# Kernel tuning notes

Hardware: AMD Instinct MI355X
Metric: run time of the kernel (lower is better)

## Reference

```python
import jax, jax.numpy as jnp
import numpy as np
from jax import lax

B, T, N, H, NC = 2, 8, 512, 64, 10
NEG = -1e9
LN_EPS = 1e-5


def _gatv2(x, mask, Wl, Wr, att, b):
    # GATv2Conv (PyG semantics, eval mode): e_ij = att . leaky_relu(Wr x_i + Wl x_j),
    # softmax over source nodes j with self-loops, out_i = sum_j alpha_ij * (Wl x_j).
    # x: (B, N, Fin); mask: (N, N) bool adjacency incl. self-loops; att: (heads, C).
    heads, C = att.shape
    Bn, Nn, _ = x.shape
    xl = (x @ Wl).reshape(Bn, Nn, heads, C)  # source transform
    xr = (x @ Wr).reshape(Bn, Nn, heads, C)  # target transform
    s = jax.nn.leaky_relu(xr[:, :, None] + xl[:, None, :], 0.2)  # (B, Ni, Nj, h, C)
    e = jnp.einsum('bijhc,hc->bijh', s, att)
    e = jnp.where(mask[None, :, :, None], e, NEG)
    alpha = jax.nn.softmax(e, axis=2)  # softmax over neighbors j
    out = jnp.einsum('bijh,bjhc->bihc', alpha, xl)
    return out.reshape(Bn, Nn, heads * C) + b


def _gru_layer(x, Wih, Whh, bih, bhh):
    # torch nn.GRU single layer, batch_first; x: (B, T, Hin)
    h0 = jnp.zeros((x.shape[0], Whh.shape[0]), x.dtype)
    def step(h, xt):
        gi = xt @ Wih + bih
        gh = h @ Whh + bhh
        ir, iz, inn = jnp.split(gi, 3, axis=-1)
        hr, hz, hn = jnp.split(gh, 3, axis=-1)
        r = jax.nn.sigmoid(ir + hr)
        z = jax.nn.sigmoid(iz + hz)
        n = jnp.tanh(inn + r * hn)
        hnew = (1.0 - z) * n + z * h
        return hnew, hnew
    _, ys = lax.scan(step, h0, jnp.swapaxes(x, 0, 1))
    return jnp.swapaxes(ys, 0, 1)


def setup_inputs() -> dict:
    key = jax.random.key(0)
    ks = jax.random.split(key, 20)
    def rn(i, shape, s=0.1):
        return jax.random.normal(ks[i], shape, jnp.float32) * s
    x_seq = jax.random.normal(ks[0], (B, T, N, 1), jnp.float32)
    a = jax.random.uniform(ks[1], (N, N))
    up = jnp.triu((a > 0.95).astype(jnp.float32), 1)
    static_adj = up + up.T  # sparse symmetric 0/1 static graph
    dyn_W = jax.random.normal(ks[2], (N, N), jnp.float32)
    reg_lambda = jnp.array([0.05], jnp.float32)
    return {
        'x_seq': x_seq, 'static_adj': static_adj, 'dyn_W': dyn_W, 'reg_lambda': reg_lambda,
        'g1_Wl': rn(3, (1, H)), 'g1_Wr': rn(4, (1, H)), 'g1_att': rn(5, (4, H // 4)), 'g1_b': jnp.zeros(H),
        'g2_Wl': rn(6, (H, H)), 'g2_Wr': rn(7, (H, H)), 'g2_att': rn(8, (1, H)), 'g2_b': jnp.zeros(H),
        'gru_Wih0': rn(9, (H, 3 * H)), 'gru_Whh0': rn(10, (H, 3 * H)), 'gru_bih0': jnp.zeros(3 * H), 'gru_bhh0': jnp.zeros(3 * H),
        'gru_Wih1': rn(11, (H, 3 * H)), 'gru_Whh1': rn(12, (H, 3 * H)), 'gru_bih1': jnp.zeros(3 * H), 'gru_bhh1': jnp.zeros(3 * H),
        'attn_W': rn(13, (H, 1)), 'attn_b': jnp.zeros(1),
        'cls_W1': rn(14, (H, H)), 'cls_b1': jnp.zeros(H), 'ln_g': jnp.ones(H), 'ln_b': jnp.zeros(H),
        'cls_W2': rn(15, (H, NC)), 'cls_b2': jnp.zeros(NC),
    }


def reference(x_seq, static_adj, dyn_W, reg_lambda,
              g1_Wl, g1_Wr, g1_att, g1_b, g2_Wl, g2_Wr, g2_att, g2_b,
              gru_Wih0, gru_Whh0, gru_bih0, gru_bhh0,
              gru_Wih1, gru_Whh1, gru_bih1, gru_bhh1,
              attn_W, attn_b, cls_W1, cls_b1, ln_g, ln_b, cls_W2, cls_b2):
    Bn, Tn, Nn, _ = x_seq.shape
    lam = jnp.maximum(reg_lambda[0], 0.01)
    t = jnp.arange(Tn, dtype=x_seq.dtype)
    gts = jnp.exp(-lam * t)  # gating values per timestep
    dyn = jax.nn.relu(dyn_W + dyn_W.T)
    fused = gts[:, None, None] * static_adj + (1.0 - gts)[:, None, None] * dyn  # (T, N, N)
    masks = (fused > 0) | jnp.eye(Nn, dtype=bool)[None]  # edge set + self-loops

    def step(carry, inp):
        xt, mask = inp  # xt: (B, N, 1)
        h = jax.nn.elu(_gatv2(xt, mask, g1_Wl, g1_Wr, g1_att, g1_b))
        h = jax.nn.elu(_gatv2(h, mask, g2_Wl, g2_Wr, g2_att, g2_b))
        return carry, h.mean(axis=1)  # (B, H) graph readout

    _, reps = lax.scan(step, 0.0, (jnp.swapaxes(x_seq, 0, 1), masks))
    h_seq = jnp.swapaxes(reps, 0, 1)  # (B, T, H)

    gru_out = _gru_layer(h_seq, gru_Wih0, gru_Whh0, gru_bih0, gru_bhh0)
    gru_out = _gru_layer(gru_out, gru_Wih1, gru_Whh1, gru_bih1, gru_bhh1)

    att_scores = jax.nn.softmax((gru_out @ attn_W + attn_b)[..., 0], axis=1)  # (B, T)
    final = jnp.einsum('bt,bth->bh', att_scores, gru_out)

    z = final @ cls_W1 + cls_b1
    mu = jnp.mean(z, axis=-1, keepdims=True)
    var = jnp.var(z, axis=-1, keepdims=True)
    z = (z - mu) / jnp.sqrt(var + LN_EPS) * ln_g + ln_b
    z = jax.nn.gelu(z, approximate=False)
    logits = z @ cls_W2 + cls_b2
    return logits, gts, att_scores
```

## Files before the change

### kernel.cpp

```cpp
#include <hip/hip_runtime.h>
#include <math.h>

#define BB 2
#define TT 8
#define NN 512
#define HH 64
#define NC 10

typedef unsigned char uchar;

__device__ __forceinline__ float elu1(float v){ return v > 0.f ? v : expm1f(v); }
__device__ __forceinline__ float sigm(float v){ return 1.f/(1.f+expf(-v)); }

__global__ __launch_bounds__(256) void k_mask(
    const float* __restrict__ dW, const float* __restrict__ sadj,
    uchar* __restrict__ M0, uchar* __restrict__ M1,
    float* __restrict__ hseq,
    const float* __restrict__ att1, const float* __restrict__ Wr1,
    const float* __restrict__ Wl1, float* __restrict__ AB,
    const float* __restrict__ Whh0, const float* __restrict__ Wih1,
    const float* __restrict__ Whh1, float4* __restrict__ WT4)
{
    __shared__ float tr[64][65];
    int bx = blockIdx.x, by = blockIdx.y;
    int tid = threadIdx.x;
    if (blockIdx.z == 1){
        int idx = (by*8 + bx)*256 + tid;
        if (idx < 3*4096){
            int m = idx >> 12, r = idx & 4095;
            int gg = r >> 6, k = r & 63;
            const float* W = (m == 0) ? Whh0 : (m == 1) ? Wih1 : Whh1;
            float4 o;
            o.x = W[k*192 + gg];
            o.y = W[k*192 + 64 + gg];
            o.z = W[k*192 + 128 + gg];
            o.w = 0.f;
            WT4[(size_t)m*4096 + r] = o;
        }
        return;
    }
    int i0 = by*64, j0 = bx*64;
    #pragma unroll
    for (int q = 0; q < 4; ++q){
        int r = (tid >> 4) + 16*q, c4 = tid & 15;
        float4 v = *(const float4*)&dW[(size_t)(j0+r)*NN + i0 + 4*c4];
        tr[r][4*c4+0] = v.x; tr[r][4*c4+1] = v.y;
        tr[r][4*c4+2] = v.z; tr[r][4*c4+3] = v.w;
    }
    __syncthreads();
    #pragma unroll
    for (int q = 0; q < 4; ++q){
        int row = (tid >> 4) + 16*q, c4 = tid & 15;
        int i = i0 + row, j = j0 + 4*c4;
        float4 d  = *(const float4*)&dW[(size_t)i*NN + j];
        float4 sa = *(const float4*)&sadj[(size_t)i*NN + j];
        uchar4 m0, m1;
        float dd0 = d.x + tr[4*c4+0][row];
        float dd1 = d.y + tr[4*c4+1][row];
        float dd2 = d.z + tr[4*c4+2][row];
        float dd3 = d.w + tr[4*c4+3][row];
        m0.x = (sa.x > 0.f) || (i == j+0);
        m0.y = (sa.y > 0.f) || (i == j+1);
        m0.z = (sa.z > 0.f) || (i == j+2);
        m0.w = (sa.w > 0.f) || (i == j+3);
        m1.x = m0.x || (dd0 > 0.f);
        m1.y = m0.y || (dd1 > 0.f);
        m1.z = m0.z || (dd2 > 0.f);
        m1.w = m0.w || (dd3 > 0.f);
        *(uchar4*)&M0[(size_t)i*NN + j] = m0;
        *(uchar4*)&M1[(size_t)i*NN + j] = m1;
    }
    int flat = (by*8 + bx)*256 + tid;
    if (flat < BB*TT*HH) hseq[flat] = 0.f;
    if (bx == 0 && by == 0 && tid < 8){
        int h = tid & 3;
        const float* W = (tid < 4) ? Wr1 : Wl1;
        float s = 0.f;
        for (int c = 0; c < 16; ++c) s += att1[h*16+c]*W[h*16+c];
        AB[tid] = s;
    }
}

__global__ __launch_bounds__(256) void k_gat1f(
    const float* __restrict__ x_seq, const uchar* __restrict__ M0,
    const uchar* __restrict__ M1,
    const float* __restrict__ Wl, const float* __restrict__ Wr,
    const float* __restrict__ att, const float* __restrict__ bias,
    const float* __restrict__ AB,
    const float* __restrict__ Wl2, const float* __restrict__ Wr2,
    const float* __restrict__ att2,
    float* __restrict__ xl2, float* __restrict__ xr2,
    float* __restrict__ ui, float* __restrict__ vj)
{
    __shared__ float x_s[NN];
    __shared__ float S_s[4][4];
    __shared__ float h_s[4][HH];
    __shared__ float Wl2_s[64*64];
    __shared__ float Wr2_s[64*64];
    int bt = blockIdx.y; int t = bt % TT;
    int i0 = blockIdx.x * 4;
    int tid = threadIdx.x;
    int il = tid >> 6, jl = tid & 63;
    int i = i0 + il;
    const uchar* M = t ? M1 : M0;
    ((float2*)x_s)[tid] = ((const float2*)(x_seq + bt*NN))[tid];
    #pragma unroll
    for (int q = 0; q < 4; ++q){
        int idx = q*256 + tid;
        ((float4*)Wl2_s)[idx] = ((const float4*)Wl2)[idx];
        ((float4*)Wr2_s)[idx] = ((const float4*)Wr2)[idx];
    }
    __syncthreads();
    float xi = x_s[i];
    const uchar* Mrow = M + (size_t)i*NN;
    float xj[8], msk[8];
    #pragma unroll
    for (int jj = 0; jj < 8; ++jj){
        int j = jj*64 + jl;
        xj[jj] = x_s[j];
        msk[jj] = Mrow[j] ? 1.f : 0.f;
    }
    float sw[4] = {0,0,0,0}, swx[4] = {0,0,0,0};
    for (int h = 0; h < 4; ++h){
        float acc[8] = {0,0,0,0,0,0,0,0};
        #pragma unroll
        for (int c = 0; c < 16; ++c){
            int hc = h*16 + c;
            float wl = Wl[hc];
            float q  = 0.4f * att[hc];
            float pr = xi * Wr[hc];
            #pragma unroll
            for (int jj = 0; jj < 8; ++jj){
                float s = fmaf(xj[jj], wl, pr);
                acc[jj] = fmaf(q, fabsf(s), acc[jj]);
            }
        }
        float lin = 0.6f * xi * AB[h];
        float al6 = 0.6f * AB[4+h];
        #pragma unroll
        for (int jj = 0; jj < 8; ++jj){
            float e = acc[jj] + fmaf(al6, xj[jj], lin);
            float w = msk[jj] * __expf(e);
            sw[h] += w;
            swx[h] = fmaf(w, xj[jj], swx[h]);
        }
    }
    #pragma unroll
    for (int off = 32; off; off >>= 1){
        #pragma unroll
        for (int h = 0; h < 4; ++h){
            sw[h]  += __shfl_down(sw[h],  off);
            swx[h] += __shfl_down(swx[h], off);
        }
    }
    if (jl == 0){
        #pragma unroll
        for (int h = 0; h < 4; ++h) S_s[il][h] = swx[h] / sw[h];
    }
    __syncthreads();
    {
        int hc = tid & 63, row = tid >> 6;
        float v = S_s[row][hc >> 4] * Wl[hc] + bias[hc];
        h_s[row][hc] = elu1(v);
    }
    __syncthreads();
    {
        int c = tid & 63, row = tid >> 6;
        float al = 0.f, ar = 0.f;
        #pragma unroll 8
        for (int k = 0; k < 64; ++k){
            float hv = h_s[row][k];
            al = fmaf(hv, Wl2_s[k*64 + c], al);
            ar = fmaf(hv, Wr2_s[k*64 + c], ar);
        }
        size_t ridx = (size_t)(bt*NN + i0 + row);
        xl2[ridx*HH + c] = al;
        xr2[ridx*HH + c] = ar;
        float a2 = att2[c];
        float pu = a2 * ar, pv = a2 * al;
        #pragma unroll
        for (int off = 32; off; off >>= 1){
            pu += __shfl_down(pu, off);
            pv += __shfl_down(pv, off);
        }
        if (c == 0){ ui[ridx] = pu; vj[ridx] = pv; }
    }
}

__global__ __launch_bounds__(512) void k_gat2(
    const float* __restrict__ xl2, const float* __restrict__ xr2,
    const uchar* __restrict__ M0, const uchar* __restrict__ M1,
    const float* __restrict__ att, const float* __restrict__ ui,
    const float* __restrict__ vj, const float* __restrict__ bias,
    float* __restrict__ hseq)
{
    __shared__ float xl_s[256][68];
    __shared__ float wT_s[256][36];
    __shared__ float v_s[256];
    __shared__ float z_s[32];

    int bt = blockIdx.y, t = bt & 7;
    int i0 = blockIdx.x * 32;
    int base = bt * NN;
    int tid = threadIdx.x;
    const uchar* M = t ? M1 : M0;

    int ig = __builtin_amdgcn_readfirstlane(tid >> 6);
    int jg = tid & 63;
    int ln = jg;
    int ig2 = ln >> 3, cg2 = ln & 7;

    const float* xrp0 = xr2 + (size_t)(base + i0 + ig*4 + 0)*HH;
    const float* xrp1 = xr2 + (size_t)(base + i0 + ig*4 + 1)*HH;
    const float* xrp2 = xr2 + (size_t)(base + i0 + ig*4 + 2)*HH;
    const float* xrp3 = xr2 + (size_t)(base + i0 + ig*4 + 3)*HH;
    float u0 = 0.6f*ui[base + i0 + ig*4 + 0];
    float u1 = 0.6f*ui[base + i0 + ig*4 + 1];
    float u2 = 0.6f*ui[base + i0 + ig*4 + 2];
    float u3 = 0.6f*ui[base + i0 + ig*4 + 3];

    float zreg[4] = {0.f,0.f,0.f,0.f};
    float acc[4][8];
    #pragma unroll
    for (int a = 0; a < 4; ++a)
        #pragma unroll
        for (int r = 0; r < 8; ++r) acc[a][r] = 0.f;

    for (int tile = 0; tile < 2; ++tile){
        int j0 = tile * 256;
        __syncthreads();
        #pragma unroll
        for (int q = 0; q < 8; ++q){
            int idx = q*512 + tid;
            int row = idx >> 4, c4 = idx & 15;
            ((float4*)&xl_s[row][0])[c4] = ((const float4*)&xl2[(size_t)(base+j0+row)*HH])[c4];
        }
        if (tid < 256) v_s[tid] = vj[base + j0 + tid];
        __syncthreads();
        float e[4][4];
        #pragma unroll
        for (int jj = 0; jj < 4; ++jj){
            float vv = 0.6f * v_s[jj*64 + jg];
            e[0][jj] = u0 + vv; e[1][jj] = u1 + vv;
            e[2][jj] = u2 + vv; e[3][jj] = u3 + vv;
        }
        #pragma unroll 4
        for (int c4 = 0; c4 < 16; ++c4){
            float4 a4 = *(const float4*)&att[c4*4];
            float qk[4];
            qk[0] = 0.4f*a4.x; qk[1] = 0.4f*a4.y; qk[2] = 0.4f*a4.z; qk[3] = 0.4f*a4.w;
            float rr[4][4];
            *(float4*)rr[0] = *(const float4*)&xrp0[c4*4];
            *(float4*)rr[1] = *(const float4*)&xrp1[c4*4];
            *(float4*)rr[2] = *(const float4*)&xrp2[c4*4];
            *(float4*)rr[3] = *(const float4*)&xrp3[c4*4];
            float xlv[4][4];
            #pragma unroll
            for (int jj = 0; jj < 4; ++jj)
                *(float4*)xlv[jj] = ((const float4*)&xl_s[jj*64+jg][0])[c4];
            #pragma unroll
            for (int jj = 0; jj < 4; ++jj)
                #pragma unroll
                for (int k = 0; k < 4; ++k){
                    float xc = xlv[jj][k];
                    #pragma unroll
                    for (int ii = 0; ii < 4; ++ii)
                        e[ii][jj] = fmaf(qk[k], fabsf(rr[ii][k] + xc), e[ii][jj]);
                }
        }
        #pragma unroll
        for (int jj = 0; jj < 4; ++jj){
            int j = jj*64 + jg;
            const uchar* mp = &M[(size_t)(i0 + ig*4)*NN + j0 + j];
            float w0 = mp[0]      ? __expf(e[0][jj]) : 0.f;
            float w1 = mp[NN]     ? __expf(e[1][jj]) : 0.f;
            float w2 = mp[2*NN]   ? __expf(e[2][jj]) : 0.f;
            float w3 = mp[3*NN]   ? __expf(e[3][jj]) : 0.f;
            zreg[0] += w0; zreg[1] += w1; zreg[2] += w2; zreg[3] += w3;
            float4 wq; wq.x = w0; wq.y = w1; wq.z = w2; wq.w = w3;
            *(float4*)&wT_s[j][ig*4] = wq;
        }
        __syncthreads();
        #pragma unroll 4
        for (int jj = 0; jj < 32; ++jj){
            int j = ig*32 + jj;
            float w4[4], xa[8];
            *(float4*)w4      = *(const float4*)&wT_s[j][ig2*4];
            *(float4*)&xa[0]  = ((const float4*)&xl_s[j][0])[cg2*2+0];
            *(float4*)&xa[4]  = ((const float4*)&xl_s[j][0])[cg2*2+1];
            #pragma unroll
            for (int a = 0; a < 4; ++a)
                #pragma unroll
                for (int r = 0; r < 8; ++r)
                    acc[a][r] = fmaf(w4[a], xa[r], acc[a][r]);
        }
    }
    __syncthreads();
    #pragma unroll
    for (int off = 32; off; off >>= 1){
        #pragma unroll
        for (int ii = 0; ii < 4; ++ii) zreg[ii] += __shfl_down(zreg[ii], off);
    }
    if (jg == 0){
        #pragma unroll
        for (int ii = 0; ii < 4; ++ii) z_s[ig*4+ii] = zreg[ii];
    }
    float* scratch = &xl_s[0][0];
    if (ig > 0){
        #pragma unroll
        for (int a = 0; a < 4; ++a)
            #pragma unroll
            for (int r = 0; r < 8; ++r)
                scratch[(a*8+r)*448 + (ig-1)*64 + ln] = acc[a][r];
    }
    __syncthreads();
    if (ig == 0){
        float pm[8];
        #pragma unroll
        for (int r = 0; r < 8; ++r) pm[r] = 0.f;
        #pragma unroll
        for (int a = 0; a < 4; ++a){
            float rz = 1.f / z_s[ig2*4 + a];
            #pragma unroll
            for (int r = 0; r < 8; ++r){
                float s = acc[a][r];
                #pragma unroll
                for (int w = 0; w < 7; ++w)
                    s += scratch[(a*8+r)*448 + w*64 + ln];
                float h = elu1(s*rz + bias[cg2*8 + r]);
                pm[r] += h;
            }
        }
        #pragma unroll
        for (int off = 32; off >= 8; off >>= 1){
            #pragma unroll
            for (int r = 0; r < 8; ++r) pm[r] += __shfl_down(pm[r], off);
        }
        if (ig2 == 0){
            #pragma unroll
            for (int r = 0; r < 8; ++r)
                atomicAdd(&hseq[bt*HH + cg2*8 + r], pm[r] * (1.f/(float)NN));
        }
    }
}

#define P4 65
__global__ __launch_bounds__(512) void k_gru2(
    const float* __restrict__ hseq, const float* __restrict__ Wih0,
    const float* __restrict__ bih0, const float4* __restrict__ WT4,
    const float* __restrict__ bhh0,
    const float* __restrict__ bih1, const float* __restrict__ bhh1,
    const float* __restrict__ lamp, const float* __restrict__ attn_W,
    const float* __restrict__ attn_b, const float* __restrict__ W1,
    const float* __restrict__ b1, const float* __restrict__ ln_g,
    const float* __restrict__ ln_b, const float* __restrict__ W2,
    const float* __restrict__ b2, float* __restrict__ out)
{
    __shared__ float4 WA[64*P4];
    __shared__ float4 WB[64*P4];
    __shared__ float gi_s[BB*TT*192];
    __shared__ float hs_s[BB*TT*HH];
    __shared__ float y_s[BB*TT*HH];
    __shared__ float sc_s[BB][TT], at_s[BB][TT];
    __shared__ float fin_s[BB][HH], z_s[BB][HH], g_s[BB][HH];
    __shared__ float mu_s[BB], iv_s[BB];
    int tid = threadIdx.x;
    int wave = tid >> 6, lane = tid & 63;
    for (int v = tid; v < 4096; v += 512){
        WA[(v >> 6)*P4 + (v & 63)] = WT4[v];
        WB[(v >> 6)*P4 + (v & 63)] = WT4[4096 + v];
    }
    for (int v = tid; v < BB*TT*HH; v += 512) hs_s[v] = hseq[v];
    __syncthreads();
    #pragma unroll
    for (int o = 0; o < 6; ++o){
        int idx = o*512 + tid;
        int b = idx / 192, g = idx % 192;
        float a = bih0[g];
        const float* hr = &hs_s[b*HH];
        #pragma unroll 8
        for (int k = 0; k < HH; ++k) a = fmaf(hr[k], Wih0[k*192 + g], a);
        gi_s[idx] = a;
    }
    __syncthreads();
    float y[TT];
    float g1r[TT], g1z[TT], g1n[TT];
    if (wave < 2){
        int b = wave;
        float bhr = bhh0[lane], bhz = bhh0[64+lane], bhn = bhh0[128+lane];
        float h = 0.f;
        for (int t = 0; t < TT; ++t){
            float ghr = bhr, ghz = bhz, ghn = bhn;
            #pragma unroll 16
            for (int k = 0; k < 64; ++k){
                float4 w4 = WA[lane*P4 + k];
                float hk = __shfl(h, k);
                ghr = fmaf(w4.x, hk, ghr);
                ghz = fmaf(w4.y, hk, ghz);
                ghn = fmaf(w4.z, hk, ghn);
            }
            const float* gi = &gi_s[(b*TT + t)*192];
            float r = sigm(gi[lane] + ghr);
            float z = sigm(gi[64+lane] + ghz);
            float n = tanhf(gi[128+lane] + r*ghn);
            h = (1.f - z)*n + z*h;
            y[t] = h;
        }
        float bi1r = bih1[lane], bi1z = bih1[64+lane], bi1n = bih1[128+lane];
        #pragma unroll
        for (int t = 0; t < TT; ++t){ g1r[t] = bi1r; g1z[t] = bi1z; g1n[t] = bi1n; }
        #pragma unroll 8
        for (int k = 0; k < 64; ++k){
            float4 w4 = WB[lane*P4 + k];
            #pragma unroll
            for (int t = 0; t < TT; ++t){
                float yk = __shfl(y[t], k);
                g1r[t] = fmaf(w4.x, yk, g1r[t]);
                g1z[t] = fmaf(w4.y, yk, g1z[t]);
                g1n[t] = fmaf(w4.z, yk, g1n[t]);
            }
        }
    }
    __syncthreads();
    if (wave >= 2){
        for (int v = tid - 128; v < 4096; v += 384)
            WA[(v >> 6)*P4 + (v & 63)] = WT4[2*4096 + v];
    }
    __syncthreads();
    if (wave < 2){
        int b = wave;
        float bhr = bhh1[lane], bhz = bhh1[64+lane], bhn = bhh1[128+lane];
        float h = 0.f;
        for (int t = 0; t < TT; ++t){
            float ghr = bhr, ghz = bhz, ghn = bhn;
            #pragma unroll 16
            for (int k = 0; k < 64; ++k){
                float4 w4 = WA[lane*P4 + k];
                float hk = __shfl(h, k);
                ghr = fmaf(w4.x, hk, ghr);
                ghz = fmaf(w4.y, hk, ghz);
                ghn = fmaf(w4.z, hk, ghn);
            }
            float r = sigm(g1r[t] + ghr);
            float z = sigm(g1z[t] + ghz);
            float n = tanhf(g1n[t] + r*ghn);
            h = (1.f - z)*n + z*h;
            y_s[(b*TT + t)*HH + lane] = h;
        }
    }
    __syncthreads();
    float lam = fmaxf(lamp[0], 0.01f);
    if (tid < TT) out[BB*NC + tid] = expf(-lam*(float)tid);
    if (tid < BB*TT){
        int bb = tid >> 3, t = tid & 7;
        float s = attn_b[0];
        const float* r = &y_s[(bb*TT+t)*HH];
        for (int h = 0; h < HH; ++h) s += r[h]*attn_W[h];
        sc_s[bb][t] = s;
    }
    __syncthreads();
    if (tid < BB){
        float mx = -INFINITY;
        for (int t = 0; t < TT; ++t) mx = fmaxf(mx, sc_s[tid][t]);
        float se = 0.f;
        for (int t = 0; t < TT; ++t){ float w = expf(sc_s[tid][t]-mx); at_s[tid][t] = w; se += w; }
        for (int t = 0; t < TT; ++t){
            at_s[tid][t] /= se;
            out[BB*NC + TT + tid*TT + t] = at_s[tid][t];
        }
    }
    __syncthreads();
    if (tid < BB*HH){
        int bb = tid >> 6, h = tid & 63;
        float a = 0.f;
        for (int t = 0; t < TT; ++t) a += at_s[bb][t]*y_s[(bb*TT+t)*HH + h];
        fin_s[bb][h] = a;
    }
    __syncthreads();
    if (tid < BB*HH){
        int bb = tid >> 6, h = tid & 63;
        float a = b1[h];
        for (int k = 0; k < HH; ++k) a += fin_s[bb][k]*W1[k*HH+h];
        z_s[bb][h] = a;
    }
    __syncthreads();
    if (tid < BB){
        float mu = 0.f;
        for (int h = 0; h < HH; ++h) mu += z_s[tid][h];
        mu *= (1.f/HH);
        float v = 0.f;
        for (int h = 0; h < HH; ++h){ float d = z_s[tid][h]-mu; v += d*d; }
        v *= (1.f/HH);
        mu_s[tid] = mu; iv_s[tid] = 1.f/sqrtf(v + 1e-5f);
    }
    __syncthreads();
    if (tid < BB*HH){
        int bb = tid >> 6, h = tid & 63;
        float zn = (z_s[bb][h]-mu_s[bb])*iv_s[bb]*ln_g[h] + ln_b[h];
        g_s[bb][h] = 0.5f*zn*(1.f + erff(zn*0.70710678118654752f));
    }
    __syncthreads();
    if (tid < BB*NC){
        int bb = tid / NC, c = tid % NC;
        float a = b2[c];
        for (int k = 0; k < HH; ++k) a += g_s[bb][k]*W2[k*NC+c];
        out[bb*NC + c] = a;
    }
}

extern "C" void kernel_launch(void* const* d_in, const int* in_sizes, int n_in,
                              void* d_out, int out_size, void* d_ws, size_t ws_size,
                              hipStream_t stream)
{
    const float* x_seq = (const float*)d_in[0];
    const float* sadj  = (const float*)d_in[1];
    const float* dynW  = (const float*)d_in[2];
    const float* lamp  = (const float*)d_in[3];
    const float* g1_Wl = (const float*)d_in[4];
    const float* g1_Wr = (const float*)d_in[5];
    const float* g1_att= (const float*)d_in[6];
    const float* g1_b  = (const float*)d_in[7];
    const float* g2_Wl = (const float*)d_in[8];
    const float* g2_Wr = (const float*)d_in[9];
    const float* g2_att= (const float*)d_in[10];
    const float* g2_b  = (const float*)d_in[11];
    const float* Wih0  = (const float*)d_in[12];
    const float* Whh0  = (const float*)d_in[13];
    const float* bih0  = (const float*)d_in[14];
    const float* bhh0  = (const float*)d_in[15];
    const float* Wih1  = (const float*)d_in[16];
    const float* Whh1  = (const float*)d_in[17];
    const float* bih1  = (const float*)d_in[18];
    const float* bhh1  = (const float*)d_in[19];
    const float* attnW = (const float*)d_in[20];
    const float* attnb = (const float*)d_in[21];
    const float* W1    = (const float*)d_in[22];
    const float* b1    = (const float*)d_in[23];
    const float* lng   = (const float*)d_in[24];
    const float* lnb   = (const float*)d_in[25];
    const float* W2    = (const float*)d_in[26];
    const float* b2    = (const float*)d_in[27];
    float* out = (float*)d_out;

    const int RWS = BB*TT*NN*HH;
    uchar* M0 = (uchar*)d_ws;
    uchar* M1 = M0 + (size_t)NN*NN;
    float* fb = (float*)(M1 + (size_t)NN*NN);
    float* AB   = fb;
    float* ui   = AB   + 16;
    float* vj   = ui   + BB*TT*NN;
    float* xl2  = vj   + BB*TT*NN;
    float* xr2  = xl2  + RWS;
    float* hseq = xr2  + RWS;
    float4* WT4 = (float4*)(hseq + BB*TT*HH);

    k_mask <<<dim3(8,8,2), 256, 0, stream>>>(dynW, sadj, M0, M1, hseq, g1_att, g1_Wr, g1_Wl, AB,
                                             Whh0, Wih1, Whh1, WT4);
    k_gat1f<<<dim3(NN/4, BB*TT), 256, 0, stream>>>(x_seq, M0, M1, g1_Wl, g1_Wr, g1_att, g1_b, AB,
                                                   g2_Wl, g2_Wr, g2_att, xl2, xr2, ui, vj);
    k_gat2 <<<dim3(NN/32, BB*TT), 512, 0, stream>>>(xl2, xr2, M0, M1, g2_att, ui, vj, g2_b, hseq);
    k_gru2 <<<1, 512, 0, stream>>>(hseq, Wih0, bih0, WT4, bhh0, bih1, bhh1,
                                   lamp, attnW, attnb, W1, b1, lng, lnb, W2, b2, out);
}
```

Measured before the change: 222.8 us.

## Split GRU recurrent matvec across two waves with register-resident weights

Each batch's hidden-to-hidden matvec is split across two waves, each holding half of the transposed Whh in registers. The hidden state is now exchanged through LDS rather than shuffles, and partial sums are combined after a block barrier. The layer-1 input projection is computed by all 512 threads reading Wih1 from global memory, instead of inside the two GRU waves. This shortens the serial per-step dependency chain and drops the LDS weight staging, at the cost of two block-wide barriers per timestep and heavier register use.

```diff
diff --git a/kernel.cpp b/kernel.cpp
--- a/kernel.cpp
+++ b/kernel.cpp
@@ -344,11 +344,10 @@
     }
 }
 
-#define P4 65
 __global__ __launch_bounds__(512) void k_gru2(
     const float* __restrict__ hseq, const float* __restrict__ Wih0,
     const float* __restrict__ bih0, const float4* __restrict__ WT4,
-    const float* __restrict__ bhh0,
+    const float* __restrict__ bhh0, const float* __restrict__ Wih1,
     const float* __restrict__ bih1, const float* __restrict__ bhh1,
     const float* __restrict__ lamp, const float* __restrict__ attn_W,
     const float* __restrict__ attn_b, const float* __restrict__ W1,
@@ -356,21 +355,27 @@
     const float* __restrict__ ln_b, const float* __restrict__ W2,
     const float* __restrict__ b2, float* __restrict__ out)
 {
-    __shared__ float4 WA[64*P4];
-    __shared__ float4 WB[64*P4];
     __shared__ float gi_s[BB*TT*192];
     __shared__ float hs_s[BB*TT*HH];
     __shared__ float y_s[BB*TT*HH];
+    __shared__ float h_lds[BB][HH];
+    __shared__ float part_s[BB][2][3][HH];
     __shared__ float sc_s[BB][TT], at_s[BB][TT];
     __shared__ float fin_s[BB][HH], z_s[BB][HH], g_s[BB][HH];
     __shared__ float mu_s[BB], iv_s[BB];
     int tid = threadIdx.x;
     int wave = tid >> 6, lane = tid & 63;
-    for (int v = tid; v < 4096; v += 512){
-        WA[(v >> 6)*P4 + (v & 63)] = WT4[v];
-        WB[(v >> 6)*P4 + (v & 63)] = WT4[4096 + v];
+    int gb = wave >> 1, half = wave & 1;
+    bool gruw = (wave < 4);
+
+    float4 Wreg[32];
+    if (gruw){
+        const float4* src = WT4 + (size_t)lane*64 + half*32;
+        #pragma unroll
+        for (int kk = 0; kk < 32; ++kk) Wreg[kk] = src[kk];
     }
     for (int v = tid; v < BB*TT*HH; v += 512) hs_s[v] = hseq[v];
+    if (tid < BB*HH) h_lds[tid >> 6][tid & 63] = 0.f;
     __syncthreads();
     #pragma unroll
     for (int o = 0; o < 6; ++o){
@@ -383,72 +388,101 @@
         gi_s[idx] = a;
     }
     __syncthreads();
-    float y[TT];
-    float g1r[TT], g1z[TT], g1n[TT];
-    if (wave < 2){
-        int b = wave;
-        float bhr = bhh0[lane], bhz = bhh0[64+lane], bhn = bhh0[128+lane];
-        float h = 0.f;
+    {
+        float bhr = 0.f, bhz = 0.f, bhn = 0.f;
+        if (gruw && half == 0){ bhr = bhh0[lane]; bhz = bhh0[64+lane]; bhn = bhh0[128+lane]; }
         for (int t = 0; t < TT; ++t){
-            float ghr = bhr, ghz = bhz, ghn = bhn;
-            #pragma unroll 16
-            for (int k = 0; k < 64; ++k){
-                float4 w4 = WA[lane*P4 + k];
-                float hk = __shfl(h, k);
-                ghr = fmaf(w4.x, hk, ghr);
-                ghz = fmaf(w4.y, hk, ghz);
-                ghn = fmaf(w4.z, hk, ghn);
+            if (gruw){
+                float hh[32];
+                #pragma unroll
+                for (int q = 0; q < 8; ++q)
+                    *(float4*)&hh[q*4] = *(const float4*)&h_lds[gb][half*32 + q*4];
+                float ar0=0,ar1=0,az0=0,az1=0,an0=0,an1=0;
+                #pragma unroll
+                for (int kk = 0; kk < 32; kk += 2){
+                    ar0 = fmaf(Wreg[kk].x,   hh[kk],   ar0);
+                    az0 = fmaf(Wreg[kk].y,   hh[kk],   az0);
+                    an0 = fmaf(Wreg[kk].z,   hh[kk],   an0);
+                    ar1 = fmaf(Wreg[kk+1].x, hh[kk+1], ar1);
+                    az1 = fmaf(Wreg[kk+1].y, hh[kk+1], az1);
+                    an1 = fmaf(Wreg[kk+1].z, hh[kk+1], an1);
+                }
+                part_s[gb][half][0][lane] = ar0 + ar1;
+                part_s[gb][half][1][lane] = az0 + az1;
+                part_s[gb][half][2][lane] = an0 + an1;
             }
-            const float* gi = &gi_s[(b*TT + t)*192];
-            float r = sigm(gi[lane] + ghr);
-            float z = sigm(gi[64+lane] + ghz);
-            float n = tanhf(gi[128+lane] + r*ghn);
-            h = (1.f - z)*n + z*h;
-            y[t] = h;
-        }
-        float bi1r = bih1[lane], bi1z = bih1[64+lane], bi1n = bih1[128+lane];
-        #pragma unroll
-        for (int t = 0; t < TT; ++t){ g1r[t] = bi1r; g1z[t] = bi1z; g1n[t] = bi1n; }
+            __syncthreads();
+            if (gruw && half == 0){
+                float ghr = part_s[gb][0][0][lane] + part_s[gb][1][0][lane] + bhr;
+                float ghz = part_s[gb][0][1][lane] + part_s[gb][1][1][lane] + bhz;
+                float ghn = part_s[gb][0][2][lane] + part_s[gb][1][2][lane] + bhn;
+                const float* gi = &gi_s[(gb*TT + t)*192];
+                float r = sigm(gi[lane] + ghr);
+                float z = sigm(gi[64+lane] + ghz);
+                float n = tanhf(gi[128+lane] + r*ghn);
+                float hn = (1.f - z)*n + z*h_lds[gb][lane];
+                h_lds[gb][lane] = hn;
+                y_s[(gb*TT + t)*HH + lane] = hn;
+            }
+            __syncthreads();
+        }
+    }
+    if (gruw){
+        const float4* src = WT4 + 2*4096 + (size_t)lane*64 + half*32;
+        #pragma unroll
+        for (int kk = 0; kk < 32; ++kk) Wreg[kk] = src[kk];
+    }
+    #pragma unroll
+    for (int o = 0; o < 6; ++o){
+        int idx = o*512 + tid;
+        int b = idx / 192, g = idx % 192;
+        float a = bih1[g];
+        const float* yr = &y_s[b*HH];
         #pragma unroll 8
-        for (int k = 0; k < 64; ++k){
-            float4 w4 = WB[lane*P4 + k];
-            #pragma unroll
-            for (int t = 0; t < TT; ++t){
-                float yk = __shfl(y[t], k);
-                g1r[t] = fmaf(w4.x, yk, g1r[t]);
-                g1z[t] = fmaf(w4.y, yk, g1z[t]);
-                g1n[t] = fmaf(w4.z, yk, g1n[t]);
+        for (int k = 0; k < HH; ++k) a = fmaf(yr[k], Wih1[k*192 + g], a);
+        gi_s[idx] = a;
+    }
+    if (tid < BB*HH) h_lds[tid >> 6][tid & 63] = 0.f;
+    __syncthreads();
+    {
+        float bhr = 0.f, bhz = 0.f, bhn = 0.f;
+        if (gruw && half == 0){ bhr = bhh1[lane]; bhz = bhh1[64+lane]; bhn = bhh1[128+lane]; }
+        for (int t = 0; t < TT; ++t){
+            if (gruw){
+                float hh[32];
+                #pragma unroll
+                for (int q = 0; q < 8; ++q)
+                    *(float4*)&hh[q*4] = *(const float4*)&h_lds[gb][half*32 + q*4];
+                float ar0=0,ar1=0,az0=0,az1=0,an0=0,an1=0;
+                #pragma unroll
+                for (int kk = 0; kk < 32; kk += 2){
+                    ar0 = fmaf(Wreg[kk].x,   hh[kk],   ar0);
+                    az0 = fmaf(Wreg[kk].y,   hh[kk],   az0);
+                    an0 = fmaf(Wreg[kk].z,   hh[kk],   an0);
+                    ar1 = fmaf(Wreg[kk+1].x, hh[kk+1], ar1);
+                    az1 = fmaf(Wreg[kk+1].y, hh[kk+1], az1);
+                    an1 = fmaf(Wreg[kk+1].z, hh[kk+1], an1);
+                }
+                part_s[gb][half][0][lane] = ar0 + ar1;
+                part_s[gb][half][1][lane] = az0 + az1;
+                part_s[gb][half][2][lane] = an0 + an1;
             }
-        }
-    }
-    __syncthreads();
-    if (wave >= 2){
-        for (int v = tid - 128; v < 4096; v += 384)
-            WA[(v >> 6)*P4 + (v & 63)] = WT4[2*4096 + v];
-    }
-    __syncthreads();
-    if (wave < 2){
-        int b = wave;
-        float bhr = bhh1[lane], bhz = bhh1[64+lane], bhn = bhh1[128+lane];
-        float h = 0.f;
-        for (int t = 0; t < TT; ++t){
-            float ghr = bhr, ghz = bhz, ghn = bhn;
-            #pragma unroll 16
-            for (int k = 0; k < 64; ++k){
-                float4 w4 = WA[lane*P4 + k];
-                float hk = __shfl(h, k);
-                ghr = fmaf(w4.x, hk, ghr);
-                ghz = fmaf(w4.y, hk, ghz);
-                ghn = fmaf(w4.z, hk, ghn);
+            __syncthreads();
+            if (gruw && half == 0){
+                float ghr = part_s[gb][0][0][lane] + part_s[gb][1][0][lane] + bhr;
+                float ghz = part_s[gb][0][1][lane] + part_s[gb][1][1][lane] + bhz;
+                float ghn = part_s[gb][0][2][lane] + part_s[gb][1][2][lane] + bhn;
+                const float* gi = &gi_s[(gb*TT + t)*192];
+                float r = sigm(gi[lane] + ghr);
+                float z = sigm(gi[64+lane] + ghz);
+                float n = tanhf(gi[128+lane] + r*ghn);
+                float hn = (1.f - z)*n + z*h_lds[gb][lane];
+                h_lds[gb][lane] = hn;
+                y_s[(gb*TT + t)*HH + lane] = hn;
             }
-            float r = sigm(g1r[t] + ghr);
-            float z = sigm(g1z[t] + ghz);
-            float n = tanhf(g1n[t] + r*ghn);
-            h = (1.f - z)*n + z*h;
-            y_s[(b*TT + t)*HH + lane] = h;
-        }
-    }
-    __syncthreads();
+            __syncthreads();
+        }
+    }
     float lam = fmaxf(lamp[0], 0.01f);
     if (tid < TT) out[BB*NC + tid] = expf(-lam*(float)tid);
     if (tid < BB*TT){
@@ -559,6 +593,6 @@
     k_gat1f<<<dim3(NN/4, BB*TT), 256, 0, stream>>>(x_seq, M0, M1, g1_Wl, g1_Wr, g1_att, g1_b, AB,
                                                    g2_Wl, g2_Wr, g2_att, xl2, xr2, ui, vj);
     k_gat2 <<<dim3(NN/32, BB*TT), 512, 0, stream>>>(xl2, xr2, M0, M1, g2_att, ui, vj, g2_b, hseq);
-    k_gru2 <<<1, 512, 0, stream>>>(hseq, Wih0, bih0, WT4, bhh0, bih1, bhh1,
+    k_gru2 <<<1, 512, 0, stream>>>(hseq, Wih0, bih0, WT4, bhh0, Wih1, bih1, bhh1,
                                    lamp, attnW, attnb, W1, b1, lng, lnb, W2, b2, out);
 }
```

Result: no change. 223.2 us (+0.2%).

## Hold GRU recurrent weights in registers and compute layer-1 input gates block-wide

Applied to the files above, without the earlier changes.

The GRU kernel now keeps each lane's 64x3 recurrent weight slice in VGPRs, loaded directly from a re-transposed global buffer, instead of reading float4 weights from padded LDS on every step. The layer-1 input projection is no longer done by two waves with shuffles. All 512 threads compute it from y_s using Wih1 straight from global memory, and the prep kernel no longer transposes Wih1. This targets LDS traffic and idle waves in the serial GRU tail, at the cost of about 192 live registers per lane and possible spilling.

```diff
diff --git a/kernel.cpp b/kernel.cpp
--- a/kernel.cpp
+++ b/kernel.cpp
@@ -18,18 +18,18 @@
     float* __restrict__ hseq,
     const float* __restrict__ att1, const float* __restrict__ Wr1,
     const float* __restrict__ Wl1, float* __restrict__ AB,
-    const float* __restrict__ Whh0, const float* __restrict__ Wih1,
-    const float* __restrict__ Whh1, float4* __restrict__ WT4)
+    const float* __restrict__ Whh0, const float* __restrict__ Whh1,
+    float4* __restrict__ WT4)
 {
     __shared__ float tr[64][65];
     int bx = blockIdx.x, by = blockIdx.y;
     int tid = threadIdx.x;
     if (blockIdx.z == 1){
         int idx = (by*8 + bx)*256 + tid;
-        if (idx < 3*4096){
+        if (idx < 2*4096){
             int m = idx >> 12, r = idx & 4095;
-            int gg = r >> 6, k = r & 63;
-            const float* W = (m == 0) ? Whh0 : (m == 1) ? Wih1 : Whh1;
+            int k = r >> 6, gg = r & 63;
+            const float* W = m ? Whh1 : Whh0;
             float4 o;
             o.x = W[k*192 + gg];
             o.y = W[k*192 + 64 + gg];
@@ -344,11 +344,10 @@
     }
 }
 
-#define P4 65
 __global__ __launch_bounds__(512) void k_gru2(
     const float* __restrict__ hseq, const float* __restrict__ Wih0,
     const float* __restrict__ bih0, const float4* __restrict__ WT4,
-    const float* __restrict__ bhh0,
+    const float* __restrict__ bhh0, const float* __restrict__ Wih1,
     const float* __restrict__ bih1, const float* __restrict__ bhh1,
     const float* __restrict__ lamp, const float* __restrict__ attn_W,
     const float* __restrict__ attn_b, const float* __restrict__ W1,
@@ -356,8 +355,6 @@
     const float* __restrict__ ln_b, const float* __restrict__ W2,
     const float* __restrict__ b2, float* __restrict__ out)
 {
-    __shared__ float4 WA[64*P4];
-    __shared__ float4 WB[64*P4];
     __shared__ float gi_s[BB*TT*192];
     __shared__ float hs_s[BB*TT*HH];
     __shared__ float y_s[BB*TT*HH];
@@ -365,87 +362,100 @@
     __shared__ float fin_s[BB][HH], z_s[BB][HH], g_s[BB][HH];
     __shared__ float mu_s[BB], iv_s[BB];
     int tid = threadIdx.x;
-    int wave = tid >> 6, lane = tid & 63;
-    for (int v = tid; v < 4096; v += 512){
-        WA[(v >> 6)*P4 + (v & 63)] = WT4[v];
-        WB[(v >> 6)*P4 + (v & 63)] = WT4[4096 + v];
+    int wave = tid >> 6, ln = tid & 63;
+    bool gw = (wave < BB);
+    int b = wave;
+
+    float wr[64], wz[64], wn[64];
+    if (gw){
+        #pragma unroll
+        for (int k = 0; k < 64; ++k){
+            float4 w4 = WT4[k*64 + ln];
+            wr[k] = w4.x; wz[k] = w4.y; wn[k] = w4.z;
+        }
     }
     for (int v = tid; v < BB*TT*HH; v += 512) hs_s[v] = hseq[v];
     __syncthreads();
     #pragma unroll
     for (int o = 0; o < 6; ++o){
         int idx = o*512 + tid;
-        int b = idx / 192, g = idx % 192;
+        int bt = idx / 192, g = idx % 192;
         float a = bih0[g];
-        const float* hr = &hs_s[b*HH];
+        const float* hr = &hs_s[bt*HH];
         #pragma unroll 8
         for (int k = 0; k < HH; ++k) a = fmaf(hr[k], Wih0[k*192 + g], a);
         gi_s[idx] = a;
     }
     __syncthreads();
-    float y[TT];
-    float g1r[TT], g1z[TT], g1n[TT];
-    if (wave < 2){
-        int b = wave;
-        float bhr = bhh0[lane], bhz = bhh0[64+lane], bhn = bhh0[128+lane];
+    if (gw){
+        float gr[TT], gz[TT], gn[TT];
+        #pragma unroll
+        for (int t = 0; t < TT; ++t){
+            gr[t] = gi_s[(b*TT+t)*192 + ln];
+            gz[t] = gi_s[(b*TT+t)*192 + 64 + ln];
+            gn[t] = gi_s[(b*TT+t)*192 + 128 + ln];
+        }
+        float bhr = bhh0[ln], bhz = bhh0[64+ln], bhn = bhh0[128+ln];
         float h = 0.f;
         for (int t = 0; t < TT; ++t){
             float ghr = bhr, ghz = bhz, ghn = bhn;
-            #pragma unroll 16
+            #pragma unroll
             for (int k = 0; k < 64; ++k){
-                float4 w4 = WA[lane*P4 + k];
                 float hk = __shfl(h, k);
-                ghr = fmaf(w4.x, hk, ghr);
-                ghz = fmaf(w4.y, hk, ghz);
-                ghn = fmaf(w4.z, hk, ghn);
+                ghr = fmaf(wr[k], hk, ghr);
+                ghz = fmaf(wz[k], hk, ghz);
+                ghn = fmaf(wn[k], hk, ghn);
             }
-            const float* gi = &gi_s[(b*TT + t)*192];
-            float r = sigm(gi[lane] + ghr);
-            float z = sigm(gi[64+lane] + ghz);
-            float n = tanhf(gi[128+lane] + r*ghn);
+            float r = sigm(gr[t] + ghr);
+            float z = sigm(gz[t] + ghz);
+            float n = tanhf(gn[t] + r*ghn);
             h = (1.f - z)*n + z*h;
-            y[t] = h;
-        }
-        float bi1r = bih1[lane], bi1z = bih1[64+lane], bi1n = bih1[128+lane];
-        #pragma unroll
-        for (int t = 0; t < TT; ++t){ g1r[t] = bi1r; g1z[t] = bi1z; g1n[t] = bi1n; }
+            y_s[(b*TT+t)*HH + ln] = h;
+        }
+    }
+    if (gw){
+        #pragma unroll
+        for (int k = 0; k < 64; ++k){
+            float4 w4 = WT4[4096 + k*64 + ln];
+            wr[k] = w4.x; wz[k] = w4.y; wn[k] = w4.z;
+        }
+    }
+    __syncthreads();
+    #pragma unroll
+    for (int o = 0; o < 6; ++o){
+        int idx = o*512 + tid;
+        int bt = idx / 192, g = idx % 192;
+        float a = bih1[g];
+        const float* yr = &y_s[bt*HH];
         #pragma unroll 8
-        for (int k = 0; k < 64; ++k){
-            float4 w4 = WB[lane*P4 + k];
-            #pragma unroll
-            for (int t = 0; t < TT; ++t){
-                float yk = __shfl(y[t], k);
-                g1r[t] = fmaf(w4.x, yk, g1r[t]);
-                g1z[t] = fmaf(w4.y, yk, g1z[t]);
-                g1n[t] = fmaf(w4.z, yk, g1n[t]);
-            }
-        }
-    }
-    __syncthreads();
-    if (wave >= 2){
-        for (int v = tid - 128; v < 4096; v += 384)
-            WA[(v >> 6)*P4 + (v & 63)] = WT4[2*4096 + v];
-    }
-    __syncthreads();
-    if (wave < 2){
-        int b = wave;
-        float bhr = bhh1[lane], bhz = bhh1[64+lane], bhn = bhh1[128+lane];
+        for (int k = 0; k < HH; ++k) a = fmaf(yr[k], Wih1[k*192 + g], a);
+        gi_s[idx] = a;
+    }
+    __syncthreads();
+    if (gw){
+        float gr[TT], gz[TT], gn[TT];
+        #pragma unroll
+        for (int t = 0; t < TT; ++t){
+            gr[t] = gi_s[(b*TT+t)*192 + ln];
+            gz[t] = gi_s[(b*TT+t)*192 + 64 + ln];
+            gn[t] = gi_s[(b*TT+t)*192 + 128 + ln];
+        }
+        float bhr = bhh1[ln], bhz = bhh1[64+ln], bhn = bhh1[128+ln];
         float h = 0.f;
         for (int t = 0; t < TT; ++t){
             float ghr = bhr, ghz = bhz, ghn = bhn;
-            #pragma unroll 16
+            #pragma unroll
             for (int k = 0; k < 64; ++k){
-                float4 w4 = WA[lane*P4 + k];
                 float hk = __shfl(h, k);
-                ghr = fmaf(w4.x, hk, ghr);
-                ghz = fmaf(w4.y, hk, ghz);
-                ghn = fmaf(w4.z, hk, ghn);
+                ghr = fmaf(wr[k], hk, ghr);
+                ghz = fmaf(wz[k], hk, ghz);
+                ghn = fmaf(wn[k], hk, ghn);
             }
-            float r = sigm(g1r[t] + ghr);
-            float z = sigm(g1z[t] + ghz);
-            float n = tanhf(g1n[t] + r*ghn);
+            float r = sigm(gr[t] + ghr);
+            float z = sigm(gz[t] + ghz);
+            float n = tanhf(gn[t] + r*ghn);
             h = (1.f - z)*n + z*h;
-            y_s[(b*TT + t)*HH + lane] = h;
+            y_s[(b*TT+t)*HH + ln] = h;
         }
     }
     __syncthreads();
@@ -555,10 +565,10 @@
     float4* WT4 = (float4*)(hseq + BB*TT*HH);
 
     k_mask <<<dim3(8,8,2), 256, 0, stream>>>(dynW, sadj, M0, M1, hseq, g1_att, g1_Wr, g1_Wl, AB,
-                                             Whh0, Wih1, Whh1, WT4);
+                                             Whh0, Whh1, WT4);
     k_gat1f<<<dim3(NN/4, BB*TT), 256, 0, stream>>>(x_seq, M0, M1, g1_Wl, g1_Wr, g1_att, g1_b, AB,
                                                    g2_Wl, g2_Wr, g2_att, xl2, xr2, ui, vj);
     k_gat2 <<<dim3(NN/32, BB*TT), 512, 0, stream>>>(xl2, xr2, M0, M1, g2_att, ui, vj, g2_b, hseq);
-    k_gru2 <<<1, 512, 0, stream>>>(hseq, Wih0, bih0, WT4, bhh0, bih1, bhh1,
+    k_gru2 <<<1, 512, 0, stream>>>(hseq, Wih0, bih0, WT4, bhh0, Wih1, bih1, bhh1,
                                    lamp, attnW, attnb, W1, b1, lng, lnb, W2, b2, out);
 }
```

After: 414.7 us. 1.86x slower.
